# Kernel tuning notes

Measured on AMD Instinct MI355X. Metric: run time of the kernel, lower is better.

Reference implementation:

```python
import jax, jax.numpy as jnp
import numpy as np

V, BLOCK, L, H, C = 50257, 1024, 4, 12, 768
HS = C // H  # 64
EPS = 1e-6  # flax LayerNorm default


def _ln(x, scale, bias):
    mu = jnp.mean(x, axis=-1, keepdims=True)
    var = jnp.var(x, axis=-1, keepdims=True)
    return (x - mu) * jax.lax.rsqrt(var + EPS) * scale + bias


def setup_inputs() -> dict:
    key = jax.random.key(0)
    ks = jax.random.split(key, 12)
    B, T = 2, 1024
    inp = {
        'idx': jax.random.randint(ks[0], (B, T), 0, V),
        'targets': jax.random.randint(ks[1], (B, T), 0, V),
        'wte': jax.random.normal(ks[2], (V, C), jnp.float32) * 0.02,
        'wpe': jax.random.normal(ks[3], (BLOCK, C), jnp.float32) * 0.02,
        'ln1_s': jnp.ones((L, C), jnp.float32),
        'ln1_b': jnp.zeros((L, C), jnp.float32),
        'attn_k': jax.random.normal(ks[4], (L, C, H, 3 * HS), jnp.float32) * 0.02,
        'attn_b': jnp.zeros((L, H, 3 * HS), jnp.float32),
        'aproj_k': jax.random.normal(ks[5], (L, C, C), jnp.float32) * 0.02,
        'aproj_b': jnp.zeros((L, C), jnp.float32),
        'ln2_s': jnp.ones((L, C), jnp.float32),
        'ln2_b': jnp.zeros((L, C), jnp.float32),
        'fc_k': jax.random.normal(ks[6], (L, C, 4 * C), jnp.float32) * 0.02,
        'fc_b': jnp.zeros((L, 4 * C), jnp.float32),
        'mproj_k': jax.random.normal(ks[7], (L, 4 * C, C), jnp.float32) * 0.02,
        'mproj_b': jnp.zeros((L, C), jnp.float32),
        'lnf_s': jnp.ones((C,), jnp.float32),
        'lnf_b': jnp.zeros((C,), jnp.float32),
    }
    return inp


def _block(x, ln1_s, ln1_b, Wqkv, bqkv, Wo, bo, ln2_s, ln2_b, Wfc, bfc, Wmp, bmp, mask):
    B, T, _ = x.shape
    h = _ln(x, ln1_s, ln1_b)
    qkv = jnp.einsum('btc,chd->bhtd', h, Wqkv) + bqkv[:, None, :]  # [B,H,T,3HS]
    q, k, v = jnp.split(qkv, 3, axis=-1)
    att = jnp.einsum('bhtd,bhsd->bhts', q, k) * (1.0 / jnp.sqrt(jnp.float32(HS)))
    att = jnp.where(mask, att, -jnp.inf)
    att = jax.nn.softmax(att, axis=-1)
    y = jnp.einsum('bhts,bhsd->bthd', att, v).reshape(B, T, C)
    x = x + y @ Wo + bo
    h = _ln(x, ln2_s, ln2_b)
    h = jax.nn.gelu(h @ Wfc + bfc, approximate=True)
    x = x + h @ Wmp + bmp
    return x


def reference(idx, targets, wte, wpe, ln1_s, ln1_b, attn_k, attn_b, aproj_k, aproj_b,
              ln2_s, ln2_b, fc_k, fc_b, mproj_k, mproj_b, lnf_s, lnf_b):
    B, T = idx.shape
    x = wte[idx] + wpe[jnp.arange(T)][None]  # [B,T,C]
    mask = jnp.tril(jnp.ones((T, T), bool))[None, None]
    for l in range(L):
        x = _block(x, ln1_s[l], ln1_b[l], attn_k[l], attn_b[l], aproj_k[l], aproj_b[l],
                   ln2_s[l], ln2_b[l], fc_k[l], fc_b[l], mproj_k[l], mproj_b[l], mask)
    x = _ln(x, lnf_s, lnf_b)
    logits = jnp.einsum('btc,vc->btv', x, wte)  # tied output projection (wte.attend)
    logp = jax.nn.log_softmax(logits, axis=-1)
    loss = -jnp.mean(jnp.take_along_axis(logp, targets[..., None], axis=-1))
    return logits, loss
```

## Files before the change

kernel.cpp:

```cpp
#include <hip/hip_runtime.h>
#include <hip/hip_bf16.h>
#include <math.h>

typedef __attribute__((ext_vector_type(8))) short bf16x8;
typedef __attribute__((ext_vector_type(4))) float f32x4;

static constexpr int Bv   = 2;
static constexpr int Tv   = 1024;
static constexpr int Cv   = 768;
static constexpr int Hv   = 12;
static constexpr int Lv   = 4;
static constexpr int Vv   = 50257;
static constexpr int Mv   = 2048;
static constexpr int NT2  = 197;
static constexpr float EPSv = 1e-6f;

__device__ __forceinline__ void gload16(const void* g, void* l) {
    __builtin_amdgcn_global_load_lds((const __attribute__((address_space(1))) void*)g,
                                     (__attribute__((address_space(3))) void*)l, 16, 0, 0);
}
template<int N>
__device__ __forceinline__ void waitvm_barrier() {
    if constexpr (N == 0)      asm volatile("s_waitcnt vmcnt(0)\ns_barrier" ::: "memory");
    else if constexpr (N == 2) asm volatile("s_waitcnt vmcnt(2)\ns_barrier" ::: "memory");
    else if constexpr (N == 3) asm volatile("s_waitcnt vmcnt(3)\ns_barrier" ::: "memory");
    else if constexpr (N == 4) asm volatile("s_waitcnt vmcnt(4)\ns_barrier" ::: "memory");
    else if constexpr (N == 6) asm volatile("s_waitcnt vmcnt(6)\ns_barrier" ::: "memory");
    else                       asm volatile("s_waitcnt vmcnt(8)\ns_barrier" ::: "memory");
}
__device__ __forceinline__ void lgkm0_barrier() {
    asm volatile("s_waitcnt lgkmcnt(0)\ns_barrier" ::: "memory");
}

__global__ void embed_kernel(const int* __restrict__ idx,
                             const float* __restrict__ wte,
                             const float* __restrict__ wpe,
                             float* __restrict__ x) {
    int row = blockIdx.x;
    int t   = row & (Tv - 1);
    int tok = idx[row];
    const float* src = wte + (size_t)tok * Cv;
    const float* pos = wpe + (size_t)t * Cv;
    float* dst = x + (size_t)row * Cv;
    for (int c = threadIdx.x; c < Cv; c += 256)
        dst[c] = src[c] + pos[c];
}

__device__ __forceinline__ ushort4 pack4bf(float4 v) {
    ushort4 u;
    u.x = __bfloat16_as_ushort(__float2bfloat16(v.x));
    u.y = __bfloat16_as_ushort(__float2bfloat16(v.y));
    u.z = __bfloat16_as_ushort(__float2bfloat16(v.z));
    u.w = __bfloat16_as_ushort(__float2bfloat16(v.w));
    return u;
}

__global__ void ln_kernel(const float* __restrict__ in,
                          const float* __restrict__ sc,
                          const float* __restrict__ bi,
                          __hip_bfloat16* __restrict__ out) {
    int row  = blockIdx.x * 4 + (threadIdx.x >> 6);
    int lane = threadIdx.x & 63;
    const float4* xr = (const float4*)(in + (size_t)row * Cv);
    float4 a = xr[lane], b = xr[lane + 64], c = xr[lane + 128];
    float sum = a.x + a.y + a.z + a.w + b.x + b.y + b.z + b.w + c.x + c.y + c.z + c.w;
    float sq  = a.x*a.x + a.y*a.y + a.z*a.z + a.w*a.w
              + b.x*b.x + b.y*b.y + b.z*b.z + b.w*b.w
              + c.x*c.x + c.y*c.y + c.z*c.z + c.w*c.w;
    #pragma unroll
    for (int off = 32; off; off >>= 1) {
        sum += __shfl_xor(sum, off, 64);
        sq  += __shfl_xor(sq,  off, 64);
    }
    float mean = sum * (1.0f / Cv);
    float var  = sq * (1.0f / Cv) - mean * mean;
    float rs   = rsqrtf(var + EPSv);
    const float4* s4 = (const float4*)sc;
    const float4* b4 = (const float4*)bi;
    ushort4* orow = (ushort4*)(out + (size_t)row * Cv);
    #pragma unroll
    for (int i = 0; i < 3; ++i) {
        float4 v = (i == 0) ? a : (i == 1) ? b : c;
        float4 s = s4[lane + 64 * i];
        float4 t = b4[lane + 64 * i];
        float4 o;
        o.x = (v.x - mean) * rs * s.x + t.x;
        o.y = (v.y - mean) * rs * s.y + t.y;
        o.z = (v.z - mean) * rs * s.z + t.z;
        o.w = (v.w - mean) * rs * s.w + t.w;
        orow[lane + 64 * i] = pack4bf(o);
    }
}

__global__ void wtrans_all_kernel(const float* __restrict__ a0, __hip_bfloat16* __restrict__ o0,
                                  const float* __restrict__ a1, __hip_bfloat16* __restrict__ o1,
                                  const float* __restrict__ a2, __hip_bfloat16* __restrict__ o2,
                                  const float* __restrict__ a3, __hip_bfloat16* __restrict__ o3) {
    __shared__ float tile[32][33];
    int bid = blockIdx.x;
    const float* in; __hip_bfloat16* out; int K, N, t;
    if (bid < 6912)       { int l = bid / 1728;          t = bid % 1728;
        in = a0 + (size_t)l * 768 * 2304; out = o0 + (size_t)l * 2304 * 768; K = 768;  N = 2304; }
    else if (bid < 9216)  { int r = bid - 6912;  int l = r / 576;  t = r % 576;
        in = a1 + (size_t)l * 768 * 768;  out = o1 + (size_t)l * 768 * 768;  K = 768;  N = 768;  }
    else if (bid < 18432) { int r = bid - 9216;  int l = r / 2304; t = r % 2304;
        in = a2 + (size_t)l * 768 * 3072; out = o2 + (size_t)l * 3072 * 768; K = 768;  N = 3072; }
    else                  { int r = bid - 18432; int l = r / 2304; t = r % 2304;
        in = a3 + (size_t)l * 3072 * 768; out = o3 + (size_t)l * 768 * 3072; K = 3072; N = 768;  }
    int nx = N / 32;
    int n0 = (t % nx) * 32, k0 = (t / nx) * 32;
    int tx = threadIdx.x & 31, ty = threadIdx.x >> 5;
    #pragma unroll
    for (int i = 0; i < 4; ++i)
        tile[ty + i * 8][tx] = in[(size_t)(k0 + ty + i * 8) * N + n0 + tx];
    __syncthreads();
    #pragma unroll
    for (int i = 0; i < 4; ++i)
        out[(size_t)(n0 + ty + i * 8) * K + k0 + tx] =
            __float2bfloat16(tile[tx][ty + i * 8]);
}

__global__ void cvt_kernel(const float* __restrict__ in,
                           __hip_bfloat16* __restrict__ out, int n4,
                           float* __restrict__ lossSlot) {
    if (blockIdx.x == 0 && threadIdx.x == 0) *lossSlot = 0.f;
    int stride = gridDim.x * 256;
    for (int i = blockIdx.x * 256 + threadIdx.x; i < n4; i += stride) {
        float4 v = ((const float4*)in)[i];
        ((ushort4*)out)[i] = pack4bf(v);
    }
}

template<int EPI, int BM>
__launch_bounds__(256)
__global__ void gemm_bf16(const __hip_bfloat16* __restrict__ A,
                          const __hip_bfloat16* __restrict__ Bt,
                          const float* __restrict__ bias,
                          const float* R, float* Cf,
                          __hip_bfloat16* __restrict__ Cb,
                          __hip_bfloat16* __restrict__ vt,
                          int M, int N, int K) {
    constexpr int FM  = BM / 32;
    constexpr int NIA = BM / 32;
    constexpr int LPT = NIA + 2;
    __shared__ __hip_bfloat16 As[2][BM * 64];
    __shared__ __hip_bfloat16 Bs[2][64 * 64];
    int tid = threadIdx.x;
    int wave = tid >> 6, lane = tid & 63;
    int wr = wave >> 1, wc = wave & 1;
    int rowBase = blockIdx.y * BM, colBase = blockIdx.x * 64;

    f32x4 acc[FM][2] = {};

    int r8 = lane >> 3;
    int cg = ((lane & 7) ^ r8) * 8;
    const __hip_bfloat16* ApS = A  + (size_t)(rowBase + wave * 8 + r8) * K + cg;
    const __hip_bfloat16* BpS = Bt + (size_t)(colBase + wave * 8 + r8) * K + cg;

    auto stage = [&](int buf, int t) {
        int k0 = t * 64;
        #pragma unroll
        for (int i = 0; i < NIA; ++i)
            gload16(ApS + (size_t)(i * 32) * K + k0, &As[buf][(i * 32 + wave * 8) * 64]);
        #pragma unroll
        for (int i = 0; i < 2; ++i)
            gload16(BpS + (size_t)(i * 32) * K + k0, &Bs[buf][(i * 32 + wave * 8) * 64]);
    };

    int fq = lane >> 4, fr = lane & 15;
    int fr7 = fr & 7;

    int nt = K / 64;
    stage(0, 0); stage(1, 1);
    waitvm_barrier<LPT>();

    for (int t = 0; t < nt; ++t) {
        int cur = t & 1;
        const __hip_bfloat16* Ab = &As[cur][0];
        const __hip_bfloat16* Bb = &Bs[cur][0];

        bf16x8 av0[FM], bv0[2];
        #pragma unroll
        for (int m = 0; m < FM; ++m)
            av0[m] = *(const bf16x8*)&Ab[(wr * (BM / 2) + m * 16 + fr) * 64 + ((fq ^ fr7) * 8)];
        #pragma unroll
        for (int n = 0; n < 2; ++n)
            bv0[n] = *(const bf16x8*)&Bb[(wc * 32 + n * 16 + fr) * 64 + ((fq ^ fr7) * 8)];
        __builtin_amdgcn_s_setprio(1);
        #pragma unroll
        for (int m = 0; m < FM; ++m)
            #pragma unroll
            for (int n = 0; n < 2; ++n)
                acc[m][n] = __builtin_amdgcn_mfma_f32_16x16x32_bf16(
                    av0[m], bv0[n], acc[m][n], 0, 0, 0);
        __builtin_amdgcn_s_setprio(0);

        bf16x8 av1[FM], bv1[2];
        #pragma unroll
        for (int m = 0; m < FM; ++m)
            av1[m] = *(const bf16x8*)&Ab[(wr * (BM / 2) + m * 16 + fr) * 64 + (((4 + fq) ^ fr7) * 8)];
        #pragma unroll
        for (int n = 0; n < 2; ++n)
            bv1[n] = *(const bf16x8*)&Bb[(wc * 32 + n * 16 + fr) * 64 + (((4 + fq) ^ fr7) * 8)];
        lgkm0_barrier();

        if (t + 2 < nt) stage(cur, t + 2);

        __builtin_amdgcn_s_setprio(1);
        #pragma unroll
        for (int m = 0; m < FM; ++m)
            #pragma unroll
            for (int n = 0; n < 2; ++n)
                acc[m][n] = __builtin_amdgcn_mfma_f32_16x16x32_bf16(
                    av1[m], bv1[n], acc[m][n], 0, 0, 0);
        __builtin_amdgcn_s_setprio(0);

        if (t + 2 < nt) waitvm_barrier<LPT>();
        else            waitvm_barrier<0>();
    }

    if (EPI == 0 && vt != nullptr && (blockIdx.x % 3) == 2) {
        __hip_bfloat16 (*Ts)[132] = (__hip_bfloat16(*)[132])&As[0][0];
        #pragma unroll
        for (int m = 0; m < FM; ++m) {
            #pragma unroll
            for (int n = 0; n < 2; ++n) {
                int dloc = wc * 32 + n * 16 + fr;
                #pragma unroll
                for (int j = 0; j < 4; ++j) {
                    int tl = wr * (BM / 2) + m * 16 + fq * 4 + j;
                    float val = acc[m][n][j] + bias[colBase + dloc];
                    Ts[dloc][tl] = __float2bfloat16(val);
                }
            }
        }
        __syncthreads();
        int h  = blockIdx.x / 3;
        int b  = rowBase >> 10;
        int bh = b * Hv + h;
        int t0 = rowBase & 1023;
        int d = tid >> 2, part = tid & 3;
        const ushort4* src = (const ushort4*)&Ts[d][part * 32];
        ushort4* dst = (ushort4*)((__hip_bfloat16*)vt +
                       ((size_t)bh * 64 + d) * Tv + t0 + part * 32);
        #pragma unroll
        for (int i = 0; i < 8; ++i) dst[i] = src[i];
        return;
    }

    #pragma unroll
    for (int m = 0; m < FM; ++m) {
        #pragma unroll
        for (int n = 0; n < 2; ++n) {
            f32x4 v = acc[m][n];
            int col = colBase + wc * 32 + n * 16 + fr;
            #pragma unroll
            for (int j = 0; j < 4; ++j) {
                int row = rowBase + wr * (BM / 2) + m * 16 + fq * 4 + j;
                float val = v[j] + bias[col];
                if (EPI == 1) {
                    val += R[(size_t)row * N + col];
                    Cf[(size_t)row * N + col] = val;
                } else {
                    if (EPI == 2) {
                        float u = val;
                        float cc = 0.7978845608028654f * (u + 0.044715f * u * u * u);
                        val = 0.5f * u * (1.0f + tanhf(cc));
                    }
                    Cb[(size_t)row * N + col] = __float2bfloat16(val);
                }
            }
        }
    }
}

__launch_bounds__(256)
__global__ void attn_kernel(const __hip_bfloat16* __restrict__ qkv,
                            const __hip_bfloat16* __restrict__ vt,
                            __hip_bfloat16* __restrict__ att) {
    __shared__ __hip_bfloat16 Qs[64 * 64];
    __shared__ __hip_bfloat16 Ks[64 * 64];
    __shared__ __hip_bfloat16 Vs[64 * 64];
    __shared__ __hip_bfloat16 Ps[64 * 64];
    int bh = blockIdx.x;
    int b = bh / Hv, h = bh % Hv;
    int qt = (int)gridDim.y - 1 - (int)blockIdx.y;
    int q0 = qt * 64;
    int tid = threadIdx.x, wave = tid >> 6, lane = tid & 63;
    int g = lane >> 4, fr = lane & 15;
    int srow8 = lane >> 3, sc8 = lane & 7;

    const __hip_bfloat16* qbase = qkv + (size_t)(b * Tv + q0) * 2304 + h * 192;
    #pragma unroll
    for (int i = 0; i < 2; ++i) {
        int row = wave * 16 + i * 8 + srow8;
        gload16(qbase + (size_t)row * 2304 + ((sc8 ^ (row & 7)) * 8),
                Qs + (wave * 16 + i * 8) * 64);
    }

    f32x4 accO[4] = {};
    float mrun[4] = {-1e30f, -1e30f, -1e30f, -1e30f};
    float lrun[4] = {0.f, 0.f, 0.f, 0.f};

    for (int kv = 0; kv <= qt; ++kv) {
        int s0 = kv * 64;
        __syncthreads();
        const __hip_bfloat16* kbase = qkv + (size_t)(b * Tv + s0) * 2304 + h * 192 + 64;
        const __hip_bfloat16* vbase = vt + (size_t)bh * 64 * Tv + s0;
        #pragma unroll
        for (int i = 0; i < 2; ++i) {
            int row = wave * 16 + i * 8 + srow8;
            gload16(kbase + (size_t)row * 2304 + ((sc8 ^ (row & 7)) * 8),
                    Ks + (wave * 16 + i * 8) * 64);
            gload16(vbase + (size_t)row * Tv + ((sc8 ^ (row & 7)) * 8),
                    Vs + (wave * 16 + i * 8) * 64);
        }
        __syncthreads();

        f32x4 s4[4] = {};
        #pragma unroll
        for (int kk = 0; kk < 2; ++kk) {
            int qrow = wave * 16 + fr;
            bf16x8 qa = *(const bf16x8*)&Qs[qrow * 64 + (((g + 4 * kk) ^ (fr & 7)) * 8)];
            #pragma unroll
            for (int n = 0; n < 4; ++n) {
                int krow = n * 16 + fr;
                bf16x8 kb = *(const bf16x8*)&Ks[krow * 64 + (((g + 4 * kk) ^ (fr & 7)) * 8)];
                s4[n] = __builtin_amdgcn_mfma_f32_16x16x32_bf16(qa, kb, s4[n], 0, 0, 0);
            }
        }

        bool dia = (kv == qt);
        #pragma unroll
        for (int j = 0; j < 4; ++j) {
            int qg = q0 + wave * 16 + g * 4 + j;
            float sj[4], mx = -1e30f;
            #pragma unroll
            for (int n = 0; n < 4; ++n) {
                float v = s4[n][j] * 0.125f;
                if (dia && (s0 + n * 16 + fr) > qg) v = -1e30f;
                sj[n] = v;
                mx = fmaxf(mx, v);
            }
            #pragma unroll
            for (int off = 1; off < 16; off <<= 1)
                mx = fmaxf(mx, __shfl_xor(mx, off, 64));
            float mnew = fmaxf(mrun[j], mx);
            float ps = 0.f;
            unsigned short pb[4];
            #pragma unroll
            for (int n = 0; n < 4; ++n) {
                float p = __expf(sj[n] - mnew);
                __hip_bfloat16 pc = __float2bfloat16(p);
                pb[n] = __bfloat16_as_ushort(pc);
                ps += __bfloat162float(pc);
            }
            #pragma unroll
            for (int off = 1; off < 16; off <<= 1)
                ps += __shfl_xor(ps, off, 64);
            float cr = __expf(mrun[j] - mnew);
            lrun[j] = lrun[j] * cr + ps;
            mrun[j] = mnew;
            int prow = wave * 16 + g * 4 + j;
            #pragma unroll
            for (int n = 0; n < 4; ++n) {
                int byteoff = (32 * n + 2 * fr) ^ ((prow & 7) << 4);
                ((unsigned short*)Ps)[prow * 64 + (byteoff >> 1)] = pb[n];
            }
            #pragma unroll
            for (int n = 0; n < 4; ++n) accO[n][j] *= cr;
        }
        __syncthreads();

        #pragma unroll
        for (int kk = 0; kk < 2; ++kk) {
            int prow = wave * 16 + fr;
            bf16x8 pa = *(const bf16x8*)&Ps[prow * 64 + (((g + 4 * kk) ^ (fr & 7)) * 8)];
            #pragma unroll
            for (int n = 0; n < 4; ++n) {
                int vrow = n * 16 + fr;
                bf16x8 vb = *(const bf16x8*)&Vs[vrow * 64 + (((g + 4 * kk) ^ (fr & 7)) * 8)];
                accO[n] = __builtin_amdgcn_mfma_f32_16x16x32_bf16(pa, vb, accO[n], 0, 0, 0);
            }
        }
    }

    #pragma unroll
    for (int j = 0; j < 4; ++j) {
        float inv = 1.0f / lrun[j];
        int row = b * Tv + q0 + wave * 16 + g * 4 + j;
        #pragma unroll
        for (int n = 0; n < 4; ++n)
            att[(size_t)row * Cv + h * 64 + n * 16 + fr] =
                __float2bfloat16(accO[n][j] * inv);
    }
}

__launch_bounds__(512, 1)
__global__ void lmhead_kernel(const __hip_bfloat16* __restrict__ A,
                              const __hip_bfloat16* __restrict__ Bt,
                              float* __restrict__ Cf,
                              float* __restrict__ pLse) {
    constexpr int K = Cv, N = Vv;
    constexpr int nt = K / 64;
    __shared__ __hip_bfloat16 As[2][16384];
    __shared__ __hip_bfloat16 Bs[2][16384];
    __shared__ float ps[4][256];

    int bid = blockIdx.x;
    int nid = (bid & 7) * NT2 + (bid >> 3);
    int rowT = nid & 7, colT = nid >> 3;
    int rowBase = rowT * 256, colBase = colT * 256;

    int tid = threadIdx.x;
    int wv = tid >> 6, lane = tid & 63;
    int wr = wv >> 2, wc = wv & 3;
    int fq = lane >> 4, fr = lane & 15;
    int fr7 = fr & 7;

    f32x4 acc[8][4] = {};

    int r8 = lane >> 3;
    int cOff = ((lane & 7) ^ r8) * 8;
    const __hip_bfloat16* ApS[4];
    const __hip_bfloat16* BpS[4];
    #pragma unroll
    for (int i = 0; i < 4; ++i) {
        int rit = wv * 32 + i * 8 + r8;
        ApS[i] = A + (size_t)(rowBase + rit) * K + cOff;
        int rb = colBase + rit;
        if (rb >= N) rb = N - 1;
        BpS[i] = Bt + (size_t)rb * K + cOff;
    }

    auto stage = [&](int buf, int tile) {
        int k0 = tile * 64;
        #pragma unroll
        for (int i = 0; i < 4; ++i)
            gload16(ApS[i] + k0, &As[buf][(wv * 4 + i) * 512]);
        #pragma unroll
        for (int i = 0; i < 4; ++i)
            gload16(BpS[i] + k0, &Bs[buf][(wv * 4 + i) * 512]);
    };

    stage(0, 0);
    stage(1, 1);
    waitvm_barrier<8>();

    for (int t = 0; t < nt; ++t) {
        int cur = t & 1;
        const __hip_bfloat16* Ab = &As[cur][0];
        const __hip_bfloat16* Bb = &Bs[cur][0];

        bf16x8 av0[8], bv0[4];
        #pragma unroll
        for (int m = 0; m < 8; ++m)
            av0[m] = *(const bf16x8*)&Ab[(wr * 128 + m * 16 + fr) * 64 + ((fq ^ fr7) * 8)];
        #pragma unroll
        for (int n = 0; n < 4; ++n)
            bv0[n] = *(const bf16x8*)&Bb[(wc * 64 + n * 16 + fr) * 64 + ((fq ^ fr7) * 8)];
        __builtin_amdgcn_s_setprio(1);
        #pragma unroll
        for (int m = 0; m < 8; ++m)
            #pragma unroll
            for (int n = 0; n < 4; ++n)
                acc[m][n] = __builtin_amdgcn_mfma_f32_16x16x32_bf16(
                    av0[m], bv0[n], acc[m][n], 0, 0, 0);
        __builtin_amdgcn_s_setprio(0);

        bf16x8 av1[8], bv1[4];
        #pragma unroll
        for (int m = 0; m < 8; ++m)
            av1[m] = *(const bf16x8*)&Ab[(wr * 128 + m * 16 + fr) * 64 + (((4 + fq) ^ fr7) * 8)];
        #pragma unroll
        for (int n = 0; n < 4; ++n)
            bv1[n] = *(const bf16x8*)&Bb[(wc * 64 + n * 16 + fr) * 64 + (((4 + fq) ^ fr7) * 8)];
        lgkm0_barrier();

        if (t + 2 < nt) stage(cur, t + 2);

        __builtin_amdgcn_s_setprio(1);
        #pragma unroll
        for (int m = 0; m < 8; ++m)
            #pragma unroll
            for (int n = 0; n < 4; ++n)
                acc[m][n] = __builtin_amdgcn_mfma_f32_16x16x32_bf16(
                    av1[m], bv1[n], acc[m][n], 0, 0, 0);
        __builtin_amdgcn_s_setprio(0);

        if (t + 2 < nt) waitvm_barrier<8>();
        else            waitvm_barrier<0>();
    }

    #pragma unroll
    for (int m = 0; m < 8; ++m) {
        #pragma unroll
        for (int j = 0; j < 4; ++j) {
            int row = rowBase + wr * 128 + m * 16 + fq * 4 + j;
            float s = 0.f;
            #pragma unroll
            for (int n = 0; n < 4; ++n) {
                int col = colBase + wc * 64 + n * 16 + fr;
                float v = acc[m][n][j];
                if (col < N) {
                    Cf[(size_t)row * N + col] = v;
                    s += __expf(v);
                }
            }
            #pragma unroll
            for (int off = 1; off < 16; off <<= 1)
                s += __shfl_xor(s, off, 64);
            if (fr == 0)
                ps[wc][wr * 128 + m * 16 + fq * 4 + j] = s;
        }
    }
    __syncthreads();
    if (tid < 256)
        pLse[(size_t)(rowBase + tid) * NT2 + colT] =
            ps[0][tid] + ps[1][tid] + ps[2][tid] + ps[3][tid];
}

__global__ void plse_reduce_kernel(const float* __restrict__ pLse,
                                   const float* __restrict__ logits,
                                   const int* __restrict__ targets,
                                   float* __restrict__ lossOut) {
    int wave = threadIdx.x >> 6;
    int row  = blockIdx.x * 4 + wave;
    int lane = threadIdx.x & 63;
    const float* pr = pLse + (size_t)row * NT2;
    float l = 0.f;
    for (int i = lane; i < NT2; i += 64) l += pr[i];
    #pragma unroll
    for (int off = 32; off; off >>= 1) l += __shfl_xor(l, off, 64);
    __shared__ float sr[4];
    if (lane == 0)
        sr[wave] = logf(l) - logits[(size_t)row * Vv + targets[row]];
    __syncthreads();
    if (threadIdx.x == 0)
        atomicAdd(lossOut, (sr[0] + sr[1] + sr[2] + sr[3]) * (1.0f / Mv));
}

extern "C" void kernel_launch(void* const* d_in, const int* in_sizes, int n_in,
                              void* d_out, int out_size, void* d_ws, size_t ws_size,
                              hipStream_t stream) {
    const int*   idx     = (const int*)  d_in[0];
    const int*   targets = (const int*)  d_in[1];
    const float* wte     = (const float*)d_in[2];
    const float* wpe     = (const float*)d_in[3];
    const float* ln1_s   = (const float*)d_in[4];
    const float* ln1_b   = (const float*)d_in[5];
    const float* attn_k  = (const float*)d_in[6];
    const float* attn_b  = (const float*)d_in[7];
    const float* aproj_k = (const float*)d_in[8];
    const float* aproj_b = (const float*)d_in[9];
    const float* ln2_s   = (const float*)d_in[10];
    const float* ln2_b   = (const float*)d_in[11];
    const float* fc_k    = (const float*)d_in[12];
    const float* fc_b    = (const float*)d_in[13];
    const float* mproj_k = (const float*)d_in[14];
    const float* mproj_b = (const float*)d_in[15];
    const float* lnf_s   = (const float*)d_in[16];
    const float* lnf_b   = (const float*)d_in[17];

    float* out = (float*)d_out;
    char* ws  = (char*)d_ws;
    char* ob  = (char*)d_out;

    constexpr size_t NEED = 81962496ULL;
    if (ws_size < NEED) return;

    __hip_bfloat16* wte_bf = (__hip_bfloat16*)(ws + 0);
    __hip_bfloat16* h_bf   = (__hip_bfloat16*)(ws + 77194752);
    float*          pLse   = (float*)(ws + 80340480);

    float*          x      = (float*)(ob + 0);
    __hip_bfloat16* qkv_bf = (__hip_bfloat16*)(ob + 6291456);
    __hip_bfloat16* vt_bf  = (__hip_bfloat16*)(ob + 15728640);
    __hip_bfloat16* att_bf = (__hip_bfloat16*)(ob + 18874368);
    __hip_bfloat16* fco_bf = (__hip_bfloat16*)(ob + 22020096);
    __hip_bfloat16* w0     = (__hip_bfloat16*)(ob + 34603008);
    __hip_bfloat16* w1     = (__hip_bfloat16*)(ob + 48758784);
    __hip_bfloat16* w2     = (__hip_bfloat16*)(ob + 53477376);
    __hip_bfloat16* w3     = (__hip_bfloat16*)(ob + 72351744);

    float* lossSlot = out + (out_size - 1);

    embed_kernel<<<Mv, 256, 0, stream>>>(idx, wte, wpe, x);

    wtrans_all_kernel<<<27648, 256, 0, stream>>>(
        attn_k, w0, aproj_k, w1, fc_k, w2, mproj_k, w3);

    for (int l = 0; l < Lv; ++l) {
        ln_kernel<<<512, 256, 0, stream>>>(x, ln1_s + l * Cv, ln1_b + l * Cv, h_bf);
        gemm_bf16<0, 128><<<dim3(36, 16), 256, 0, stream>>>(
            h_bf, w0 + (size_t)l * 2304 * Cv, attn_b + l * 2304, nullptr, nullptr,
            qkv_bf, vt_bf, Mv, 2304, Cv);
        attn_kernel<<<dim3(24, 16), 256, 0, stream>>>(qkv_bf, vt_bf, att_bf);
        gemm_bf16<1, 64><<<dim3(12, 32), 256, 0, stream>>>(
            att_bf, w1 + (size_t)l * Cv * Cv, aproj_b + l * Cv, x, x, nullptr,
            nullptr, Mv, Cv, Cv);
        ln_kernel<<<512, 256, 0, stream>>>(x, ln2_s + l * Cv, ln2_b + l * Cv, h_bf);
        gemm_bf16<2, 128><<<dim3(48, 16), 256, 0, stream>>>(
            h_bf, w2 + (size_t)l * 3072 * Cv, fc_b + l * 3072, nullptr, nullptr,
            fco_bf, nullptr, Mv, 3072, Cv);
        gemm_bf16<1, 64><<<dim3(12, 32), 256, 0, stream>>>(
            fco_bf, w3 + (size_t)l * Cv * 3072, mproj_b + l * Cv, x, x, nullptr,
            nullptr, Mv, Cv, 3072);
    }

    ln_kernel<<<512, 256, 0, stream>>>(x, lnf_s, lnf_b, h_bf);
    cvt_kernel<<<2048, 256, 0, stream>>>(wte, wte_bf, (Vv * Cv) / 4, lossSlot);
    lmhead_kernel<<<8 * NT2, 512, 0, stream>>>(h_bf, wte_bf, out, pLse);
    plse_reduce_kernel<<<512, 256, 0, stream>>>(pLse, out, targets, lossSlot);
}
```

Measured before the change: 878.9 us.

## Halve lm-head K-tile to raise occupancy and fold wte conversion into weight transpose

The lm-head GEMM now stages 32-wide K tiles instead of 64, halving its shared memory, using a new 4-slot XOR swizzle, and declaring launch bounds of 4 blocks per CU so more workgroups can be resident. The separate wte fp32-to-bf16 conversion kernel is merged into the weight-transpose launch as extra blocks, which removes one launch and lets it overlap with transposes. The risks are twice as many barrier and wait steps per K and register pressure from the 128 accumulator values under the tighter launch bound, which could cause spills.

```diff
diff --git a/kernel.cpp b/kernel.cpp
--- a/kernel.cpp
+++ b/kernel.cpp
@@ -95,9 +95,22 @@
 __global__ void wtrans_all_kernel(const float* __restrict__ a0, __hip_bfloat16* __restrict__ o0,
                                   const float* __restrict__ a1, __hip_bfloat16* __restrict__ o1,
                                   const float* __restrict__ a2, __hip_bfloat16* __restrict__ o2,
-                                  const float* __restrict__ a3, __hip_bfloat16* __restrict__ o3) {
+                                  const float* __restrict__ a3, __hip_bfloat16* __restrict__ o3,
+                                  const float* __restrict__ wte, __hip_bfloat16* __restrict__ wte_bf,
+                                  float* __restrict__ lossSlot) {
+    int bid = blockIdx.x;
+    if (bid >= 27648) {
+        int cb = bid - 27648;
+        if (cb == 0 && threadIdx.x == 0) *lossSlot = 0.f;
+        int n4 = (Vv * Cv) / 4;
+        int stride = 4736 * 256;
+        for (int i = cb * 256 + threadIdx.x; i < n4; i += stride) {
+            float4 v = ((const float4*)wte)[i];
+            ((ushort4*)wte_bf)[i] = pack4bf(v);
+        }
+        return;
+    }
     __shared__ float tile[32][33];
-    int bid = blockIdx.x;
     const float* in; __hip_bfloat16* out; int K, N, t;
     if (bid < 6912)       { int l = bid / 1728;          t = bid % 1728;
         in = a0 + (size_t)l * 768 * 2304; out = o0 + (size_t)l * 2304 * 768; K = 768;  N = 2304; }
@@ -118,17 +131,6 @@
     for (int i = 0; i < 4; ++i)
         out[(size_t)(n0 + ty + i * 8) * K + k0 + tx] =
             __float2bfloat16(tile[tx][ty + i * 8]);
-}
-
-__global__ void cvt_kernel(const float* __restrict__ in,
-                           __hip_bfloat16* __restrict__ out, int n4,
-                           float* __restrict__ lossSlot) {
-    if (blockIdx.x == 0 && threadIdx.x == 0) *lossSlot = 0.f;
-    int stride = gridDim.x * 256;
-    for (int i = blockIdx.x * 256 + threadIdx.x; i < n4; i += stride) {
-        float4 v = ((const float4*)in)[i];
-        ((ushort4*)out)[i] = pack4bf(v);
-    }
 }
 
 template<int EPI, int BM>
@@ -396,15 +398,15 @@
     }
 }
 
-__launch_bounds__(512, 1)
+__launch_bounds__(512, 4)
 __global__ void lmhead_kernel(const __hip_bfloat16* __restrict__ A,
                               const __hip_bfloat16* __restrict__ Bt,
                               float* __restrict__ Cf,
                               float* __restrict__ pLse) {
     constexpr int K = Cv, N = Vv;
-    constexpr int nt = K / 64;
-    __shared__ __hip_bfloat16 As[2][16384];
-    __shared__ __hip_bfloat16 Bs[2][16384];
+    constexpr int nt = K / 32;
+    __shared__ __hip_bfloat16 As[2][8192];
+    __shared__ __hip_bfloat16 Bs[2][8192];
     __shared__ float ps[4][256];
 
     int bid = blockIdx.x;
@@ -416,17 +418,18 @@
     int wv = tid >> 6, lane = tid & 63;
     int wr = wv >> 2, wc = wv & 3;
     int fq = lane >> 4, fr = lane & 15;
-    int fr7 = fr & 7;
+    int slot0 = (fq ^ fr ^ (fr >> 2)) & 3;
 
     f32x4 acc[8][4] = {};
 
-    int r8 = lane >> 3;
-    int cOff = ((lane & 7) ^ r8) * 8;
-    const __hip_bfloat16* ApS[4];
-    const __hip_bfloat16* BpS[4];
-    #pragma unroll
-    for (int i = 0; i < 4; ++i) {
-        int rit = wv * 32 + i * 8 + r8;
+    int rl   = lane >> 2;
+    int swzr = (rl ^ (rl >> 2)) & 3;
+    int cOff = ((lane & 3) ^ swzr) * 8;
+    const __hip_bfloat16* ApS[2];
+    const __hip_bfloat16* BpS[2];
+    #pragma unroll
+    for (int i = 0; i < 2; ++i) {
+        int rit = wv * 32 + i * 16 + rl;
         ApS[i] = A + (size_t)(rowBase + rit) * K + cOff;
         int rb = colBase + rit;
         if (rb >= N) rb = N - 1;
@@ -434,61 +437,45 @@
     }
 
     auto stage = [&](int buf, int tile) {
-        int k0 = tile * 64;
-        #pragma unroll
-        for (int i = 0; i < 4; ++i)
-            gload16(ApS[i] + k0, &As[buf][(wv * 4 + i) * 512]);
-        #pragma unroll
-        for (int i = 0; i < 4; ++i)
-            gload16(BpS[i] + k0, &Bs[buf][(wv * 4 + i) * 512]);
+        int k0 = tile * 32;
+        #pragma unroll
+        for (int i = 0; i < 2; ++i)
+            gload16(ApS[i] + k0, &As[buf][(wv * 32 + i * 16) * 32]);
+        #pragma unroll
+        for (int i = 0; i < 2; ++i)
+            gload16(BpS[i] + k0, &Bs[buf][(wv * 32 + i * 16) * 32]);
     };
 
     stage(0, 0);
     stage(1, 1);
-    waitvm_barrier<8>();
+    waitvm_barrier<4>();
 
     for (int t = 0; t < nt; ++t) {
         int cur = t & 1;
         const __hip_bfloat16* Ab = &As[cur][0];
         const __hip_bfloat16* Bb = &Bs[cur][0];
 
-        bf16x8 av0[8], bv0[4];
+        bf16x8 av[8], bv[4];
         #pragma unroll
         for (int m = 0; m < 8; ++m)
-            av0[m] = *(const bf16x8*)&Ab[(wr * 128 + m * 16 + fr) * 64 + ((fq ^ fr7) * 8)];
+            av[m] = *(const bf16x8*)&Ab[(wr * 128 + m * 16 + fr) * 32 + slot0 * 8];
         #pragma unroll
         for (int n = 0; n < 4; ++n)
-            bv0[n] = *(const bf16x8*)&Bb[(wc * 64 + n * 16 + fr) * 64 + ((fq ^ fr7) * 8)];
+            bv[n] = *(const bf16x8*)&Bb[(wc * 64 + n * 16 + fr) * 32 + slot0 * 8];
+        lgkm0_barrier();
+
+        if (t + 2 < nt) stage(cur, t + 2);
+
         __builtin_amdgcn_s_setprio(1);
         #pragma unroll
         for (int m = 0; m < 8; ++m)
             #pragma unroll
             for (int n = 0; n < 4; ++n)
                 acc[m][n] = __builtin_amdgcn_mfma_f32_16x16x32_bf16(
-                    av0[m], bv0[n], acc[m][n], 0, 0, 0);
+                    av[m], bv[n], acc[m][n], 0, 0, 0);
         __builtin_amdgcn_s_setprio(0);
 
-        bf16x8 av1[8], bv1[4];
-        #pragma unroll
-        for (int m = 0; m < 8; ++m)
-            av1[m] = *(const bf16x8*)&Ab[(wr * 128 + m * 16 + fr) * 64 + (((4 + fq) ^ fr7) * 8)];
-        #pragma unroll
-        for (int n = 0; n < 4; ++n)
-            bv1[n] = *(const bf16x8*)&Bb[(wc * 64 + n * 16 + fr) * 64 + (((4 + fq) ^ fr7) * 8)];
-        lgkm0_barrier();
-
-        if (t + 2 < nt) stage(cur, t + 2);
-
-        __builtin_amdgcn_s_setprio(1);
-        #pragma unroll
-        for (int m = 0; m < 8; ++m)
-            #pragma unroll
-            for (int n = 0; n < 4; ++n)
-                acc[m][n] = __builtin_amdgcn_mfma_f32_16x16x32_bf16(
-                    av1[m], bv1[n], acc[m][n], 0, 0, 0);
-        __builtin_amdgcn_s_setprio(0);
-
-        if (t + 2 < nt) waitvm_barrier<8>();
+        if (t + 2 < nt) waitvm_barrier<4>();
         else            waitvm_barrier<0>();
     }
 
@@ -587,8 +574,8 @@
 
     embed_kernel<<<Mv, 256, 0, stream>>>(idx, wte, wpe, x);
 
-    wtrans_all_kernel<<<27648, 256, 0, stream>>>(
-        attn_k, w0, aproj_k, w1, fc_k, w2, mproj_k, w3);
+    wtrans_all_kernel<<<32384, 256, 0, stream>>>(
+        attn_k, w0, aproj_k, w1, fc_k, w2, mproj_k, w3, wte, wte_bf, lossSlot);
 
     for (int l = 0; l < Lv; ++l) {
         ln_kernel<<<512, 256, 0, stream>>>(x, ln1_s + l * Cv, ln1_b + l * Cv, h_bf);
@@ -609,7 +596,6 @@
     }
 
     ln_kernel<<<512, 256, 0, stream>>>(x, lnf_s, lnf_b, h_bf);
-    cvt_kernel<<<2048, 256, 0, stream>>>(wte, wte_bf, (Vv * Cv) / 4, lossSlot);
     lmhead_kernel<<<8 * NT2, 512, 0, stream>>>(h_bf, wte_bf, out, pLse);
     plse_reduce_kernel<<<512, 256, 0, stream>>>(pLse, out, targets, lossSlot);
 }
```

New measurement: 2.389 ms. +171.8%, slower.
